# Kernel tuning notes

Measured on AMD Instinct MI355X. Metric: run time of the kernel, lower is better.

## Reference

```python
import jax, jax.numpy as jnp
import numpy as np

N = 50000   # nodes
E = 800000  # edges (avg degree 16)
D = 64      # feature dim (input_dim == hidden_dim == output_dim for num_layer=2)
BN_EPS = 1e-5


def setup_inputs() -> dict:
    key = jax.random.key(0)
    ks = jax.random.split(key, 8)
    def lin_w(k, fan_in, fan_out):
        return jax.random.normal(k, (fan_in, fan_out), jnp.float32) / np.sqrt(fan_in).astype(np.float32)
    inp = {
        "x": jax.random.normal(ks[0], (N, D), jnp.float32),
        "edge_index": jax.random.randint(ks[1], (2, E), 0, N),
    }
    ki = 2
    for l in range(2):
        for s in ("a", "b"):
            inp[f"w{l}{s}"] = lin_w(ks[ki], D, D)
            inp[f"b{l}{s}"] = jnp.zeros((D,), jnp.float32)
            inp[f"g{l}{s}"] = jnp.ones((D,), jnp.float32)   # BN gamma
            inp[f"be{l}{s}"] = jnp.zeros((D,), jnp.float32)  # BN beta
            ki += 1
    inp["lin_w"] = lin_w(ks[6], 2 * D, D)  # JK cat of 2 layers -> 2D, final lin -> D
    inp["lin_b"] = jnp.zeros((D,), jnp.float32)
    return inp


def _bn(h, g, b):
    # BatchNorm1d in training mode: batch statistics over the node axis
    m = h.mean(axis=0)
    v = h.var(axis=0)
    return (h - m) * jax.lax.rsqrt(v + BN_EPS) * g + b


def _gin(h, src, dst, w1, b1, g1, be1, w2, b2, g2, be2):
    # GINConv with eps=0: (1+eps)*x_i + sum_{j->i} x_j, then MLP(Lin-BN-ReLU-Lin-BN-ReLU)
    agg = jax.ops.segment_sum(h[src], dst, num_segments=N) + h
    h = jax.nn.relu(_bn(agg @ w1 + b1, g1, be1))
    return jax.nn.relu(_bn(h @ w2 + b2, g2, be2))


def reference(x, edge_index, w0a, b0a, g0a, be0a, w0b, b0b, g0b, be0b,
              w1a, b1a, g1a, be1a, w1b, b1b, g1b, be1b, lin_w, lin_b):
    src, dst = edge_index[0], edge_index[1]
    h1 = _gin(x, src, dst, w0a, b0a, g0a, be0a, w0b, b0b, g0b, be0b)
    h2 = _gin(h1, src, dst, w1a, b1a, g1a, be1a, w1b, b1b, g1b, be1b)
    # JumpingKnowledge 'cat' over the conv outputs (res[1:]), then final linear
    return jnp.concatenate([h1, h2], axis=1) @ lin_w + lin_b
```

## Files before the change

kernel.cpp:

```cpp
#include <hip/hip_runtime.h>
#include <hip/hip_bf16.h>

#define NN 50000
#define NE 800000
#define BN_EPS 1e-5f
#define CHUNK 8192
#define NCH 98
#define NBK 196

typedef __attribute__((ext_vector_type(4))) float f32x4;
typedef __attribute__((ext_vector_type(4))) short s16x4;

__device__ __forceinline__ float bf2f(__hip_bfloat16 v) { return __bfloat162float(v); }

__global__ void zero_k(int* __restrict__ p, int n) {
    int i = blockIdx.x * 256 + threadIdx.x;
    if (i < n) p[i] = 0;
}

__global__ void cvt_k(const float* __restrict__ X, __hip_bfloat16* __restrict__ Xb) {
    int i = blockIdx.x * 256 + threadIdx.x;
    if (i < NN * 16) {
        f32x4 v = *(const f32x4*)(X + (size_t)i * 4);
        s16x4 ov;
        #pragma unroll
        for (int j = 0; j < 4; j++) {
            __hip_bfloat16 b = __float2bfloat16(v[j]);
            ov[j] = __builtin_bit_cast(short, b);
        }
        *(s16x4*)((short*)Xb + (size_t)i * 4) = ov;
    }
}

__global__ void bhist_k(const int* __restrict__ dst, int* __restrict__ bcnt) {
    __shared__ int c[256];
    int t = threadIdx.x;
    c[t] = 0;
    __syncthreads();
    int base = blockIdx.x * CHUNK;
    int n = NE - base; if (n > CHUNK) n = CHUNK;
    for (int i = t; i < n; i += 256) atomicAdd(&c[dst[base + i] >> 8], 1);
    __syncthreads();
    if (c[t]) atomicAdd(&bcnt[t], c[t]);
}

__global__ void bscan_k(const int* __restrict__ bcnt, int* __restrict__ bbase,
                        int* __restrict__ bres, int* __restrict__ off) {
    __shared__ int s[256];
    int t = threadIdx.x;
    int v = bcnt[t];
    s[t] = v;
    __syncthreads();
    for (int d = 1; d < 256; d <<= 1) {
        int u = (t >= d) ? s[t - d] : 0;
        __syncthreads();
        s[t] += u;
        __syncthreads();
    }
    int ex = s[t] - v;
    bbase[t] = ex;
    bres[t] = ex;
    if (t == 0) { bbase[256] = NE; off[NN] = NE; }
}

__global__ void bscatter_k(const int* __restrict__ src, const int* __restrict__ dst,
                           int* __restrict__ bres, int* __restrict__ ebuf) {
    __shared__ int cnt[256], loff[256], lcur[256], gst[256], sc[256];
    __shared__ int packed[CHUNK];
    int t = threadIdx.x;
    cnt[t] = 0;
    __syncthreads();
    int base = blockIdx.x * CHUNK;
    int n = NE - base; if (n > CHUNK) n = CHUNK;
    for (int i = t; i < n; i += 256) atomicAdd(&cnt[dst[base + i] >> 8], 1);
    __syncthreads();
    sc[t] = cnt[t];
    __syncthreads();
    for (int d = 1; d < 256; d <<= 1) {
        int u = (t >= d) ? sc[t - d] : 0;
        __syncthreads();
        sc[t] += u;
        __syncthreads();
    }
    loff[t] = sc[t] - cnt[t];
    lcur[t] = loff[t];
    __syncthreads();
    for (int i = t; i < n; i += 256) {
        int d = dst[base + i];
        int b = d >> 8;
        int p = atomicAdd(&lcur[b], 1);
        packed[p] = src[base + i] | ((d & 255) << 16) | (b << 24);
    }
    __syncthreads();
    if (cnt[t]) gst[t] = atomicAdd(&bres[t], cnt[t]);
    __syncthreads();
    for (int i = t; i < n; i += 256) {
        int v = packed[i];
        int b = (v >> 24) & 255;
        ebuf[gst[b] + i - loff[b]] = v & 0xFFFFFF;
    }
}

__global__ void csr_k(const int* __restrict__ bbase, const int* __restrict__ ebuf,
                      int* __restrict__ off, int* __restrict__ adj) {
    __shared__ int cnt[256], loff[256], lcur[256], sc[256];
    int b = blockIdx.x, t = threadIdx.x;
    int s0 = bbase[b], s1 = bbase[b + 1];
    int n = s1 - s0;
    cnt[t] = 0;
    __syncthreads();
    for (int i = t; i < n; i += 256) atomicAdd(&cnt[(ebuf[s0 + i] >> 16) & 255], 1);
    __syncthreads();
    sc[t] = cnt[t];
    __syncthreads();
    for (int d = 1; d < 256; d <<= 1) {
        int u = (t >= d) ? sc[t - d] : 0;
        __syncthreads();
        sc[t] += u;
        __syncthreads();
    }
    loff[t] = sc[t] - cnt[t];
    lcur[t] = loff[t];
    int node = b * 256 + t;
    if (node < NN) off[node] = s0 + loff[t];
    __syncthreads();
    for (int i = t; i < n; i += 256) {
        int v = ebuf[s0 + i];
        int p = atomicAdd(&lcur[(v >> 16) & 255], 1);
        adj[s0 + p] = v & 0xFFFF;
    }
}

__global__ void gather_k(const __hip_bfloat16* __restrict__ X,
                         const int* __restrict__ off, const int* __restrict__ adj,
                         float* __restrict__ AGG) {
    int node = blockIdx.x * 4 + (threadIdx.x >> 6);
    int lane = threadIdx.x & 63;
    if (node >= NN) return;
    float acc = bf2f(X[(size_t)node * 64 + lane]);
    int s = off[node], e = off[node + 1];
    int p = s;
    for (; p + 8 <= e; p += 8) {
        int j0 = adj[p + 0], j1 = adj[p + 1], j2 = adj[p + 2], j3 = adj[p + 3];
        int j4 = adj[p + 4], j5 = adj[p + 5], j6 = adj[p + 6], j7 = adj[p + 7];
        float v0 = bf2f(X[(size_t)j0 * 64 + lane]);
        float v1 = bf2f(X[(size_t)j1 * 64 + lane]);
        float v2 = bf2f(X[(size_t)j2 * 64 + lane]);
        float v3 = bf2f(X[(size_t)j3 * 64 + lane]);
        float v4 = bf2f(X[(size_t)j4 * 64 + lane]);
        float v5 = bf2f(X[(size_t)j5 * 64 + lane]);
        float v6 = bf2f(X[(size_t)j6 * 64 + lane]);
        float v7 = bf2f(X[(size_t)j7 * 64 + lane]);
        acc += ((v0 + v1) + (v2 + v3)) + ((v4 + v5) + (v6 + v7));
    }
    if (p + 4 <= e) {
        int j0 = adj[p + 0], j1 = adj[p + 1], j2 = adj[p + 2], j3 = adj[p + 3];
        float v0 = bf2f(X[(size_t)j0 * 64 + lane]);
        float v1 = bf2f(X[(size_t)j1 * 64 + lane]);
        float v2 = bf2f(X[(size_t)j2 * 64 + lane]);
        float v3 = bf2f(X[(size_t)j3 * 64 + lane]);
        acc += (v0 + v1) + (v2 + v3);
        p += 4;
    }
    for (; p < e; p++) acc += bf2f(X[(size_t)adj[p] * 64 + lane]);
    AGG[(size_t)node * 64 + lane] = acc;
}

__global__ void gemm64_k(const float* __restrict__ A,
                         const float* __restrict__ W,
                         const float* __restrict__ bias,
                         float* __restrict__ T,
                         float* __restrict__ sums) {
    __shared__ float As[64 * 72];
    __shared__ float Ws[64 * 64];
    __shared__ float lsum[64], lssq[64];
    int tid = threadIdx.x;
    int rowbase = blockIdx.x * 64;
    for (int i = tid; i < 64 * 16; i += 256) {
        int r = i >> 4, kq = i & 15;
        int row = rowbase + r;
        if (row >= NN) row = NN - 1;
        f32x4 v = *(const f32x4*)(A + (size_t)row * 64 + kq * 4);
        #pragma unroll
        for (int q = 0; q < 4; q++) As[(kq * 4 + q) * 72 + r] = v[q];
    }
    for (int i = tid; i < 1024; i += 256) {
        *(f32x4*)(Ws + i * 4) = *(const f32x4*)(W + i * 4);
    }
    if (tid < 64) { lsum[tid] = 0.f; lssq[tid] = 0.f; }
    __syncthreads();

    int ty = tid >> 4, tx = tid & 15;
    float acc[4][4] = {};
    for (int k = 0; k < 64; k++) {
        float a[4], wv[4];
        #pragma unroll
        for (int i = 0; i < 4; i++) a[i] = As[k * 72 + ty * 4 + i];
        #pragma unroll
        for (int j = 0; j < 4; j++) wv[j] = Ws[k * 64 + tx * 4 + j];
        #pragma unroll
        for (int i = 0; i < 4; i++)
            #pragma unroll
            for (int j = 0; j < 4; j++) acc[i][j] += a[i] * wv[j];
    }

    f32x4 bv = *(const f32x4*)(bias + tx * 4);
    float ps[4] = {0.f, 0.f, 0.f, 0.f}, pq[4] = {0.f, 0.f, 0.f, 0.f};
    #pragma unroll
    for (int i = 0; i < 4; i++) {
        int row = rowbase + ty * 4 + i;
        if (row < NN) {
            f32x4 v;
            #pragma unroll
            for (int j = 0; j < 4; j++) {
                v[j] = acc[i][j] + bv[j];
                ps[j] += v[j];
                pq[j] += v[j] * v[j];
            }
            *(f32x4*)(T + (size_t)row * 64 + tx * 4) = v;
        }
    }
    #pragma unroll
    for (int j = 0; j < 4; j++) {
        atomicAdd(&lsum[tx * 4 + j], ps[j]);
        atomicAdd(&lssq[tx * 4 + j], pq[j]);
    }
    __syncthreads();
    if (tid < 64) {
        atomicAdd(&sums[tid], lsum[tid]);
        atomicAdd(&sums[64 + tid], lssq[tid]);
    }
}

__global__ void gemm64bn_k(const float* __restrict__ Tin,
                           const float* __restrict__ stats,
                           const float* __restrict__ g,
                           const float* __restrict__ be,
                           const float* __restrict__ W,
                           const float* __restrict__ bias,
                           float* __restrict__ T,
                           float* __restrict__ sums) {
    __shared__ float As[64 * 72];
    __shared__ float Ws[64 * 64];
    __shared__ float sc[64], sh[64];
    __shared__ float lsum[64], lssq[64];
    int tid = threadIdx.x;
    int rowbase = blockIdx.x * 64;
    if (tid < 64) {
        float m = stats[tid] * (1.0f / NN);
        float var = stats[64 + tid] * (1.0f / NN) - m * m;
        if (var < 0.f) var = 0.f;
        float s = g[tid] * rsqrtf(var + BN_EPS);
        sc[tid] = s;
        sh[tid] = be[tid] - m * s;
        lsum[tid] = 0.f;
        lssq[tid] = 0.f;
    }
    __syncthreads();
    for (int i = tid; i < 64 * 16; i += 256) {
        int r = i >> 4, kq = i & 15;
        int row = rowbase + r;
        if (row >= NN) row = NN - 1;
        f32x4 v = *(const f32x4*)(Tin + (size_t)row * 64 + kq * 4);
        #pragma unroll
        for (int q = 0; q < 4; q++) {
            int k = kq * 4 + q;
            float u = v[q] * sc[k] + sh[k];
            As[k * 72 + r] = u > 0.f ? u : 0.f;
        }
    }
    for (int i = tid; i < 1024; i += 256) {
        *(f32x4*)(Ws + i * 4) = *(const f32x4*)(W + i * 4);
    }
    __syncthreads();

    int ty = tid >> 4, tx = tid & 15;
    float acc[4][4] = {};
    for (int k = 0; k < 64; k++) {
        float a[4], wv[4];
        #pragma unroll
        for (int i = 0; i < 4; i++) a[i] = As[k * 72 + ty * 4 + i];
        #pragma unroll
        for (int j = 0; j < 4; j++) wv[j] = Ws[k * 64 + tx * 4 + j];
        #pragma unroll
        for (int i = 0; i < 4; i++)
            #pragma unroll
            for (int j = 0; j < 4; j++) acc[i][j] += a[i] * wv[j];
    }

    f32x4 bv = *(const f32x4*)(bias + tx * 4);
    float ps[4] = {0.f, 0.f, 0.f, 0.f}, pq[4] = {0.f, 0.f, 0.f, 0.f};
    #pragma unroll
    for (int i = 0; i < 4; i++) {
        int row = rowbase + ty * 4 + i;
        if (row < NN) {
            f32x4 v;
            #pragma unroll
            for (int j = 0; j < 4; j++) {
                v[j] = acc[i][j] + bv[j];
                ps[j] += v[j];
                pq[j] += v[j] * v[j];
            }
            *(f32x4*)(T + (size_t)row * 64 + tx * 4) = v;
        }
    }
    #pragma unroll
    for (int j = 0; j < 4; j++) {
        atomicAdd(&lsum[tx * 4 + j], ps[j]);
        atomicAdd(&lssq[tx * 4 + j], pq[j]);
    }
    __syncthreads();
    if (tid < 64) {
        atomicAdd(&sums[tid], lsum[tid]);
        atomicAdd(&sums[64 + tid], lssq[tid]);
    }
}

__global__ void bn_k(const float* __restrict__ T, const float* __restrict__ sums,
                     const float* __restrict__ g,
                     const float* __restrict__ be,
                     float* __restrict__ H, __hip_bfloat16* __restrict__ Hb) {
    __shared__ float sc[64], sh[64];
    int tid = threadIdx.x;
    if (tid < 64) {
        float m = sums[tid] * (1.0f / NN);
        float var = sums[64 + tid] * (1.0f / NN) - m * m;
        if (var < 0.f) var = 0.f;
        float s = g[tid] * rsqrtf(var + BN_EPS);
        sc[tid] = s;
        sh[tid] = be[tid] - m * s;
    }
    __syncthreads();
    int i = blockIdx.x * 256 + tid;
    if (i < NN * 16) {
        int row = i >> 4, f = (i & 15) * 4;
        f32x4 v = *(const f32x4*)(T + (size_t)row * 64 + f);
        f32x4 u;
        s16x4 ub;
        #pragma unroll
        for (int j = 0; j < 4; j++) {
            float w = v[j] * sc[f + j] + sh[f + j];
            u[j] = w > 0.f ? w : 0.f;
            __hip_bfloat16 b = __float2bfloat16(u[j]);
            ub[j] = __builtin_bit_cast(short, b);
        }
        *(f32x4*)(H + (size_t)row * 64 + f) = u;
        *(s16x4*)((short*)Hb + (size_t)row * 64 + f) = ub;
    }
}

__global__ void gemmfin2_k(const float* __restrict__ H1,
                           const float* __restrict__ T2,
                           const float* __restrict__ stats,
                           const float* __restrict__ g,
                           const float* __restrict__ be,
                           const float* __restrict__ W,
                           const float* __restrict__ bias,
                           float* __restrict__ O) {
    __shared__ float As[128 * 72];
    __shared__ float Ws[128 * 64];
    __shared__ float sc[64], sh[64];
    int tid = threadIdx.x;
    int rowbase = blockIdx.x * 64;
    if (tid < 64) {
        float m = stats[tid] * (1.0f / NN);
        float var = stats[64 + tid] * (1.0f / NN) - m * m;
        if (var < 0.f) var = 0.f;
        float s = g[tid] * rsqrtf(var + BN_EPS);
        sc[tid] = s;
        sh[tid] = be[tid] - m * s;
    }
    __syncthreads();
    for (int i = tid; i < 64 * 16; i += 256) {
        int r = i >> 4, kq = i & 15;
        int row = rowbase + r;
        if (row >= NN) row = NN - 1;
        f32x4 v1 = *(const f32x4*)(H1 + (size_t)row * 64 + kq * 4);
        f32x4 v2 = *(const f32x4*)(T2 + (size_t)row * 64 + kq * 4);
        #pragma unroll
        for (int q = 0; q < 4; q++) {
            int k = kq * 4 + q;
            As[k * 72 + r] = v1[q];
            float u = v2[q] * sc[k] + sh[k];
            As[(64 + k) * 72 + r] = u > 0.f ? u : 0.f;
        }
    }
    for (int i = tid; i < 2048; i += 256) {
        *(f32x4*)(Ws + i * 4) = *(const f32x4*)(W + i * 4);
    }
    __syncthreads();

    int ty = tid >> 4, tx = tid & 15;
    float acc[4][4] = {};
    for (int k = 0; k < 128; k++) {
        float a[4], wv[4];
        #pragma unroll
        for (int i = 0; i < 4; i++) a[i] = As[k * 72 + ty * 4 + i];
        #pragma unroll
        for (int j = 0; j < 4; j++) wv[j] = Ws[k * 64 + tx * 4 + j];
        #pragma unroll
        for (int i = 0; i < 4; i++)
            #pragma unroll
            for (int j = 0; j < 4; j++) acc[i][j] += a[i] * wv[j];
    }

    f32x4 bv = *(const f32x4*)(bias + tx * 4);
    #pragma unroll
    for (int i = 0; i < 4; i++) {
        int row = rowbase + ty * 4 + i;
        if (row < NN) {
            f32x4 v;
            #pragma unroll
            for (int j = 0; j < 4; j++) v[j] = acc[i][j] + bv[j];
            *(f32x4*)(O + (size_t)row * 64 + tx * 4) = v;
        }
    }
}

extern "C" void kernel_launch(void* const* d_in, const int* in_sizes, int n_in,
                              void* d_out, int out_size, void* d_ws, size_t ws_size,
                              hipStream_t stream) {
    const float* x   = (const float*)d_in[0];
    const int*   ei  = (const int*)d_in[1];
    const float* w0a = (const float*)d_in[2];
    const float* b0a = (const float*)d_in[3];
    const float* g0a = (const float*)d_in[4];
    const float* be0a= (const float*)d_in[5];
    const float* w0b = (const float*)d_in[6];
    const float* b0b = (const float*)d_in[7];
    const float* g0b = (const float*)d_in[8];
    const float* be0b= (const float*)d_in[9];
    const float* w1a = (const float*)d_in[10];
    const float* b1a = (const float*)d_in[11];
    const float* g1a = (const float*)d_in[12];
    const float* be1a= (const float*)d_in[13];
    const float* w1b = (const float*)d_in[14];
    const float* b1b = (const float*)d_in[15];
    const float* g1b = (const float*)d_in[16];
    const float* be1b= (const float*)d_in[17];
    const float* lw  = (const float*)d_in[18];
    const float* lb  = (const float*)d_in[19];
    float* out = (float*)d_out;
    (void)in_sizes; (void)n_in; (void)out_size; (void)ws_size;

    char* wsb = (char*)d_ws;
    size_t o = 0;
    auto alloc = [&](size_t bytes) -> char* {
        char* p = wsb + o;
        o += (bytes + 255) & ~(size_t)255;
        return p;
    };
    int* bcnt = (int*)alloc(256 * 4);
    float* sums = (float*)alloc(512 * 4);
    int* bbase = (int*)alloc(257 * 4);
    int* bres = (int*)alloc(256 * 4);
    int* off = (int*)alloc((NN + 1) * 4);
    int* adj = (int*)alloc(NE * 4);
    int* ebuf = (int*)alloc(NE * 4);
    float* AGG = (float*)alloc((size_t)NN * 64 * 4);
    float* T   = (float*)alloc((size_t)NN * 64 * 4);
    float* T2  = (float*)alloc((size_t)NN * 64 * 4);
    float* HC  = (float*)alloc((size_t)NN * 64 * 4);
    __hip_bfloat16* Xb  = (__hip_bfloat16*)alloc((size_t)NN * 64 * 2);
    __hip_bfloat16* HCb = (__hip_bfloat16*)alloc((size_t)NN * 64 * 2);

    const int* src = ei;
    const int* dst = ei + NE;

    zero_k<<<3, 256, 0, stream>>>((int*)d_ws, 768);
    bhist_k<<<NCH, 256, 0, stream>>>(dst, bcnt);
    bscan_k<<<1, 256, 0, stream>>>(bcnt, bbase, bres, off);
    bscatter_k<<<NCH, 256, 0, stream>>>(src, dst, bres, ebuf);
    csr_k<<<NBK, 256, 0, stream>>>(bbase, ebuf, off, adj);

    const int ggrid = NN / 4;
    const int mgrid = (NN + 63) / 64;
    const int agrid = (NN * 16 + 255) / 256;

    cvt_k<<<agrid, 256, 0, stream>>>(x, Xb);

    gather_k<<<ggrid, 256, 0, stream>>>(Xb, off, adj, AGG);
    gemm64_k<<<mgrid, 256, 0, stream>>>(AGG, w0a, b0a, T, sums + 0);
    gemm64bn_k<<<mgrid, 256, 0, stream>>>(T, sums + 0, g0a, be0a, w0b, b0b, T2, sums + 128);
    bn_k<<<agrid, 256, 0, stream>>>(T2, sums + 128, g0b, be0b, HC, HCb);

    gather_k<<<ggrid, 256, 0, stream>>>(HCb, off, adj, AGG);
    gemm64_k<<<mgrid, 256, 0, stream>>>(AGG, w1a, b1a, T, sums + 256);
    gemm64bn_k<<<mgrid, 256, 0, stream>>>(T, sums + 256, g1a, be1a, w1b, b1b, T2, sums + 384);

    gemmfin2_k<<<mgrid, 256, 0, stream>>>(HC, T2, sums + 384, g1b, be1b, lw, lb, out);
}
```

Baseline: 355.2 us.

## Use bf16 MFMA for dense GEMMs and merge preprocessing kernels

Replaces the fp32 LDS-tiled GEMMs with bf16 MFMA 16x16x32 instructions that read operands directly from global memory, using weights pre-transposed to bf16. The aggregation output and the layer-1 hidden state are stored in bf16 instead of fp32, which cuts memory traffic. Histogram, feature conversion and weight conversion are merged into one prep kernel with per-chunk partial counts, which removes the zeroing kernel and the global atomics. The cost is lower precision in the GEMM inputs, and the output stores are now scalar and strided rather than vectorized.

```diff
diff --git a/kernel.cpp b/kernel.cpp
--- a/kernel.cpp
+++ b/kernel.cpp
@@ -4,51 +4,72 @@
 #define NN 50000
 #define NE 800000
 #define BN_EPS 1e-5f
-#define CHUNK 8192
-#define NCH 98
+#define CHUNK 4096
+#define NCH 196
 #define NBK 196
 
 typedef __attribute__((ext_vector_type(4))) float f32x4;
+typedef __attribute__((ext_vector_type(8))) short s16x8;
 typedef __attribute__((ext_vector_type(4))) short s16x4;
 
 __device__ __forceinline__ float bf2f(__hip_bfloat16 v) { return __bfloat162float(v); }
-
-__global__ void zero_k(int* __restrict__ p, int n) {
-    int i = blockIdx.x * 256 + threadIdx.x;
-    if (i < n) p[i] = 0;
-}
-
-__global__ void cvt_k(const float* __restrict__ X, __hip_bfloat16* __restrict__ Xb) {
-    int i = blockIdx.x * 256 + threadIdx.x;
-    if (i < NN * 16) {
-        f32x4 v = *(const f32x4*)(X + (size_t)i * 4);
-        s16x4 ov;
-        #pragma unroll
-        for (int j = 0; j < 4; j++) {
-            __hip_bfloat16 b = __float2bfloat16(v[j]);
-            ov[j] = __builtin_bit_cast(short, b);
-        }
-        *(s16x4*)((short*)Xb + (size_t)i * 4) = ov;
-    }
-}
-
-__global__ void bhist_k(const int* __restrict__ dst, int* __restrict__ bcnt) {
-    __shared__ int c[256];
-    int t = threadIdx.x;
-    c[t] = 0;
-    __syncthreads();
-    int base = blockIdx.x * CHUNK;
-    int n = NE - base; if (n > CHUNK) n = CHUNK;
-    for (int i = t; i < n; i += 256) atomicAdd(&c[dst[base + i] >> 8], 1);
-    __syncthreads();
-    if (c[t]) atomicAdd(&bcnt[t], c[t]);
-}
-
-__global__ void bscan_k(const int* __restrict__ bcnt, int* __restrict__ bbase,
-                        int* __restrict__ bres, int* __restrict__ off) {
+__device__ __forceinline__ short f2bs(float v) {
+    __hip_bfloat16 b = __float2bfloat16(v);
+    return __builtin_bit_cast(short, b);
+}
+
+__global__ void prep_k(const int* __restrict__ dst, int* __restrict__ part,
+                       const float* __restrict__ x, __hip_bfloat16* __restrict__ Xb,
+                       const float* __restrict__ w0a, const float* __restrict__ w0b,
+                       const float* __restrict__ w1a, const float* __restrict__ w1b,
+                       const float* __restrict__ lw,
+                       short* __restrict__ Wt0a, short* __restrict__ Wt0b,
+                       short* __restrict__ Wt1a, short* __restrict__ Wt1b,
+                       short* __restrict__ Wtf) {
+    int b = blockIdx.x, t = threadIdx.x;
+    if (b < NCH) {
+        __shared__ int c[256];
+        c[t] = 0;
+        __syncthreads();
+        int base = b * CHUNK;
+        int n = NE - base; if (n > CHUNK) n = CHUNK;
+        for (int i = t; i < n; i += 256) atomicAdd(&c[dst[base + i] >> 8], 1);
+        __syncthreads();
+        part[b * 256 + t] = c[t];
+    } else if (b < 196 + 3125) {
+        int i = (b - 196) * 256 + t;
+        if (i < NN * 16) {
+            f32x4 v = *(const f32x4*)(x + (size_t)i * 4);
+            s16x4 ov;
+            #pragma unroll
+            for (int j = 0; j < 4; j++) ov[j] = f2bs(v[j]);
+            *(s16x4*)((short*)Xb + (size_t)i * 4) = ov;
+        }
+    } else {
+        int wb = b - 3321;
+        if (wb < 4) {
+            const float* W = wb == 0 ? w0a : wb == 1 ? w0b : wb == 2 ? w1a : w1b;
+            short* Wt = wb == 0 ? Wt0a : wb == 1 ? Wt0b : wb == 2 ? Wt1a : Wt1b;
+            for (int e = t; e < 4096; e += 256) {
+                int k = e >> 6, n = e & 63;
+                Wt[n * 64 + k] = f2bs(W[e]);
+            }
+        } else {
+            for (int e = t; e < 8192; e += 256) {
+                int k = e >> 6, n = e & 63;
+                Wtf[n * 128 + k] = f2bs(lw[e]);
+            }
+        }
+    }
+}
+
+__global__ void bscan_k(const int* __restrict__ part, int* __restrict__ bbase,
+                        int* __restrict__ bres, int* __restrict__ off,
+                        float* __restrict__ sums) {
     __shared__ int s[256];
     int t = threadIdx.x;
-    int v = bcnt[t];
+    int v = 0;
+    for (int c = 0; c < NCH; c++) v += part[c * 256 + t];
     s[t] = v;
     __syncthreads();
     for (int d = 1; d < 256; d <<= 1) {
@@ -61,6 +82,7 @@
     bbase[t] = ex;
     bres[t] = ex;
     if (t == 0) { bbase[256] = NE; off[NN] = NE; }
+    sums[t] = 0.f; sums[256 + t] = 0.f;
 }
 
 __global__ void bscatter_k(const int* __restrict__ src, const int* __restrict__ dst,
@@ -133,7 +155,7 @@
 
 __global__ void gather_k(const __hip_bfloat16* __restrict__ X,
                          const int* __restrict__ off, const int* __restrict__ adj,
-                         float* __restrict__ AGG) {
+                         __hip_bfloat16* __restrict__ AGG) {
     int node = blockIdx.x * 4 + (threadIdx.x >> 6);
     int lane = threadIdx.x & 63;
     if (node >= NN) return;
@@ -163,67 +185,54 @@
         p += 4;
     }
     for (; p < e; p++) acc += bf2f(X[(size_t)adj[p] * 64 + lane]);
-    AGG[(size_t)node * 64 + lane] = acc;
-}
-
-__global__ void gemm64_k(const float* __restrict__ A,
-                         const float* __restrict__ W,
+    AGG[(size_t)node * 64 + lane] = __float2bfloat16(acc);
+}
+
+
+__global__ void gemm_a_k(const __hip_bfloat16* __restrict__ Ab,
+                         const short* __restrict__ Wt,
                          const float* __restrict__ bias,
                          float* __restrict__ T,
                          float* __restrict__ sums) {
-    __shared__ float As[64 * 72];
-    __shared__ float Ws[64 * 64];
     __shared__ float lsum[64], lssq[64];
     int tid = threadIdx.x;
-    int rowbase = blockIdx.x * 64;
-    for (int i = tid; i < 64 * 16; i += 256) {
-        int r = i >> 4, kq = i & 15;
-        int row = rowbase + r;
-        if (row >= NN) row = NN - 1;
-        f32x4 v = *(const f32x4*)(A + (size_t)row * 64 + kq * 4);
+    if (tid < 64) { lsum[tid] = 0.f; lssq[tid] = 0.f; }
+    __syncthreads();
+    int wv = tid >> 6, L = tid & 63;
+    int m = L & 15, quad = L >> 4;
+    int wrow = blockIdx.x * 64 + wv * 16;
+    int arow = wrow + m;
+    if (arow >= NN) arow = NN - 1;
+    const short* Ap = (const short*)Ab;
+    s16x8 a0 = *(const s16x8*)(Ap + (size_t)arow * 64 + quad * 8);
+    s16x8 a1 = *(const s16x8*)(Ap + (size_t)arow * 64 + 32 + quad * 8);
+    f32x4 acc[4];
+    #pragma unroll
+    for (int nt = 0; nt < 4; nt++) {
+        int n = nt * 16 + m;
+        s16x8 b0 = *(const s16x8*)(Wt + n * 64 + quad * 8);
+        s16x8 b1 = *(const s16x8*)(Wt + n * 64 + 32 + quad * 8);
+        acc[nt] = (f32x4){0.f, 0.f, 0.f, 0.f};
+        acc[nt] = __builtin_amdgcn_mfma_f32_16x16x32_bf16(a0, b0, acc[nt], 0, 0, 0);
+        acc[nt] = __builtin_amdgcn_mfma_f32_16x16x32_bf16(a1, b1, acc[nt], 0, 0, 0);
+    }
+    #pragma unroll
+    for (int nt = 0; nt < 4; nt++) {
+        int col = nt * 16 + m;
+        float bv = bias[col];
+        float ps = 0.f, pq = 0.f;
         #pragma unroll
-        for (int q = 0; q < 4; q++) As[(kq * 4 + q) * 72 + r] = v[q];
-    }
-    for (int i = tid; i < 1024; i += 256) {
-        *(f32x4*)(Ws + i * 4) = *(const f32x4*)(W + i * 4);
-    }
-    if (tid < 64) { lsum[tid] = 0.f; lssq[tid] = 0.f; }
-    __syncthreads();
-
-    int ty = tid >> 4, tx = tid & 15;
-    float acc[4][4] = {};
-    for (int k = 0; k < 64; k++) {
-        float a[4], wv[4];
-        #pragma unroll
-        for (int i = 0; i < 4; i++) a[i] = As[k * 72 + ty * 4 + i];
-        #pragma unroll
-        for (int j = 0; j < 4; j++) wv[j] = Ws[k * 64 + tx * 4 + j];
-        #pragma unroll
-        for (int i = 0; i < 4; i++)
-            #pragma unroll
-            for (int j = 0; j < 4; j++) acc[i][j] += a[i] * wv[j];
-    }
-
-    f32x4 bv = *(const f32x4*)(bias + tx * 4);
-    float ps[4] = {0.f, 0.f, 0.f, 0.f}, pq[4] = {0.f, 0.f, 0.f, 0.f};
-    #pragma unroll
-    for (int i = 0; i < 4; i++) {
-        int row = rowbase + ty * 4 + i;
-        if (row < NN) {
-            f32x4 v;
-            #pragma unroll
-            for (int j = 0; j < 4; j++) {
-                v[j] = acc[i][j] + bv[j];
-                ps[j] += v[j];
-                pq[j] += v[j] * v[j];
+        for (int r = 0; r < 4; r++) {
+            int orow = wrow + quad * 4 + r;
+            if (orow < NN) {
+                float v = acc[nt][r] + bv;
+                T[(size_t)orow * 64 + col] = v;
+                ps += v;
+                pq += v * v;
             }
-            *(f32x4*)(T + (size_t)row * 64 + tx * 4) = v;
-        }
-    }
-    #pragma unroll
-    for (int j = 0; j < 4; j++) {
-        atomicAdd(&lsum[tx * 4 + j], ps[j]);
-        atomicAdd(&lssq[tx * 4 + j], pq[j]);
+        }
+        atomicAdd(&lsum[col], ps);
+        atomicAdd(&lssq[col], pq);
     }
     __syncthreads();
     if (tid < 64) {
@@ -232,82 +241,70 @@
     }
 }
 
-__global__ void gemm64bn_k(const float* __restrict__ Tin,
-                           const float* __restrict__ stats,
-                           const float* __restrict__ g,
-                           const float* __restrict__ be,
-                           const float* __restrict__ W,
-                           const float* __restrict__ bias,
-                           float* __restrict__ T,
-                           float* __restrict__ sums) {
-    __shared__ float As[64 * 72];
-    __shared__ float Ws[64 * 64];
-    __shared__ float sc[64], sh[64];
-    __shared__ float lsum[64], lssq[64];
+__global__ void gemm_bn_k(const float* __restrict__ Tin,
+                          const float* __restrict__ stats,
+                          const float* __restrict__ g, const float* __restrict__ be,
+                          const short* __restrict__ Wt,
+                          const float* __restrict__ bias,
+                          float* __restrict__ T,
+                          float* __restrict__ sums) {
+    __shared__ float sc[64], sh[64], lsum[64], lssq[64];
     int tid = threadIdx.x;
-    int rowbase = blockIdx.x * 64;
     if (tid < 64) {
-        float m = stats[tid] * (1.0f / NN);
-        float var = stats[64 + tid] * (1.0f / NN) - m * m;
+        float mm = stats[tid] * (1.0f / NN);
+        float var = stats[64 + tid] * (1.0f / NN) - mm * mm;
         if (var < 0.f) var = 0.f;
         float s = g[tid] * rsqrtf(var + BN_EPS);
         sc[tid] = s;
-        sh[tid] = be[tid] - m * s;
-        lsum[tid] = 0.f;
-        lssq[tid] = 0.f;
-    }
-    __syncthreads();
-    for (int i = tid; i < 64 * 16; i += 256) {
-        int r = i >> 4, kq = i & 15;
-        int row = rowbase + r;
-        if (row >= NN) row = NN - 1;
-        f32x4 v = *(const f32x4*)(Tin + (size_t)row * 64 + kq * 4);
+        sh[tid] = be[tid] - mm * s;
+        lsum[tid] = 0.f; lssq[tid] = 0.f;
+    }
+    __syncthreads();
+    int wv = tid >> 6, L = tid & 63;
+    int m = L & 15, quad = L >> 4;
+    int wrow = blockIdx.x * 64 + wv * 16;
+    int arow = wrow + m;
+    if (arow >= NN) arow = NN - 1;
+    f32x4 t0 = *(const f32x4*)(Tin + (size_t)arow * 64 + quad * 8);
+    f32x4 t1 = *(const f32x4*)(Tin + (size_t)arow * 64 + quad * 8 + 4);
+    f32x4 t2 = *(const f32x4*)(Tin + (size_t)arow * 64 + 32 + quad * 8);
+    f32x4 t3 = *(const f32x4*)(Tin + (size_t)arow * 64 + 32 + quad * 8 + 4);
+    s16x8 a0, a1;
+    #pragma unroll
+    for (int j = 0; j < 4; j++) {
+        int k0 = quad * 8 + j, k1 = quad * 8 + 4 + j;
+        float u0 = t0[j] * sc[k0] + sh[k0]; a0[j]     = f2bs(u0 > 0.f ? u0 : 0.f);
+        float u1 = t1[j] * sc[k1] + sh[k1]; a0[4 + j] = f2bs(u1 > 0.f ? u1 : 0.f);
+        float u2 = t2[j] * sc[32 + k0] + sh[32 + k0]; a1[j]     = f2bs(u2 > 0.f ? u2 : 0.f);
+        float u3 = t3[j] * sc[32 + k1] + sh[32 + k1]; a1[4 + j] = f2bs(u3 > 0.f ? u3 : 0.f);
+    }
+    f32x4 acc[4];
+    #pragma unroll
+    for (int nt = 0; nt < 4; nt++) {
+        int n = nt * 16 + m;
+        s16x8 b0 = *(const s16x8*)(Wt + n * 64 + quad * 8);
+        s16x8 b1 = *(const s16x8*)(Wt + n * 64 + 32 + quad * 8);
+        acc[nt] = (f32x4){0.f, 0.f, 0.f, 0.f};
+        acc[nt] = __builtin_amdgcn_mfma_f32_16x16x32_bf16(a0, b0, acc[nt], 0, 0, 0);
+        acc[nt] = __builtin_amdgcn_mfma_f32_16x16x32_bf16(a1, b1, acc[nt], 0, 0, 0);
+    }
+    #pragma unroll
+    for (int nt = 0; nt < 4; nt++) {
+        int col = nt * 16 + m;
+        float bv = bias[col];
+        float ps = 0.f, pq = 0.f;
         #pragma unroll
-        for (int q = 0; q < 4; q++) {
-            int k = kq * 4 + q;
-            float u = v[q] * sc[k] + sh[k];
-            As[k * 72 + r] = u > 0.f ? u : 0.f;
-        }
-    }
-    for (int i = tid; i < 1024; i += 256) {
-        *(f32x4*)(Ws + i * 4) = *(const f32x4*)(W + i * 4);
-    }
-    __syncthreads();
-
-    int ty = tid >> 4, tx = tid & 15;
-    float acc[4][4] = {};
-    for (int k = 0; k < 64; k++) {
-        float a[4], wv[4];
-        #pragma unroll
-        for (int i = 0; i < 4; i++) a[i] = As[k * 72 + ty * 4 + i];
-        #pragma unroll
-        for (int j = 0; j < 4; j++) wv[j] = Ws[k * 64 + tx * 4 + j];
-        #pragma unroll
-        for (int i = 0; i < 4; i++)
-            #pragma unroll
-            for (int j = 0; j < 4; j++) acc[i][j] += a[i] * wv[j];
-    }
-
-    f32x4 bv = *(const f32x4*)(bias + tx * 4);
-    float ps[4] = {0.f, 0.f, 0.f, 0.f}, pq[4] = {0.f, 0.f, 0.f, 0.f};
-    #pragma unroll
-    for (int i = 0; i < 4; i++) {
-        int row = rowbase + ty * 4 + i;
-        if (row < NN) {
-            f32x4 v;
-            #pragma unroll
-            for (int j = 0; j < 4; j++) {
-                v[j] = acc[i][j] + bv[j];
-                ps[j] += v[j];
-                pq[j] += v[j] * v[j];
+        for (int r = 0; r < 4; r++) {
+            int orow = wrow + quad * 4 + r;
+            if (orow < NN) {
+                float v = acc[nt][r] + bv;
+                T[(size_t)orow * 64 + col] = v;
+                ps += v;
+                pq += v * v;
             }
-            *(f32x4*)(T + (size_t)row * 64 + tx * 4) = v;
-        }
-    }
-    #pragma unroll
-    for (int j = 0; j < 4; j++) {
-        atomicAdd(&lsum[tx * 4 + j], ps[j]);
-        atomicAdd(&lssq[tx * 4 + j], pq[j]);
+        }
+        atomicAdd(&lsum[col], ps);
+        atomicAdd(&lssq[col], pq);
     }
     __syncthreads();
     if (tid < 64) {
@@ -317,9 +314,8 @@
 }
 
 __global__ void bn_k(const float* __restrict__ T, const float* __restrict__ sums,
-                     const float* __restrict__ g,
-                     const float* __restrict__ be,
-                     float* __restrict__ H, __hip_bfloat16* __restrict__ Hb) {
+                     const float* __restrict__ g, const float* __restrict__ be,
+                     __hip_bfloat16* __restrict__ Hb) {
     __shared__ float sc[64], sh[64];
     int tid = threadIdx.x;
     if (tid < 64) {
@@ -335,84 +331,77 @@
     if (i < NN * 16) {
         int row = i >> 4, f = (i & 15) * 4;
         f32x4 v = *(const f32x4*)(T + (size_t)row * 64 + f);
-        f32x4 u;
         s16x4 ub;
         #pragma unroll
         for (int j = 0; j < 4; j++) {
             float w = v[j] * sc[f + j] + sh[f + j];
-            u[j] = w > 0.f ? w : 0.f;
-            __hip_bfloat16 b = __float2bfloat16(u[j]);
-            ub[j] = __builtin_bit_cast(short, b);
-        }
-        *(f32x4*)(H + (size_t)row * 64 + f) = u;
+            ub[j] = f2bs(w > 0.f ? w : 0.f);
+        }
         *(s16x4*)((short*)Hb + (size_t)row * 64 + f) = ub;
     }
 }
 
-__global__ void gemmfin2_k(const float* __restrict__ H1,
+__global__ void gemm_fin_k(const __hip_bfloat16* __restrict__ H1b,
                            const float* __restrict__ T2,
                            const float* __restrict__ stats,
-                           const float* __restrict__ g,
-                           const float* __restrict__ be,
-                           const float* __restrict__ W,
+                           const float* __restrict__ g, const float* __restrict__ be,
+                           const short* __restrict__ Wtf,
                            const float* __restrict__ bias,
                            float* __restrict__ O) {
-    __shared__ float As[128 * 72];
-    __shared__ float Ws[128 * 64];
     __shared__ float sc[64], sh[64];
     int tid = threadIdx.x;
-    int rowbase = blockIdx.x * 64;
     if (tid < 64) {
-        float m = stats[tid] * (1.0f / NN);
-        float var = stats[64 + tid] * (1.0f / NN) - m * m;
+        float mm = stats[tid] * (1.0f / NN);
+        float var = stats[64 + tid] * (1.0f / NN) - mm * mm;
         if (var < 0.f) var = 0.f;
         float s = g[tid] * rsqrtf(var + BN_EPS);
         sc[tid] = s;
-        sh[tid] = be[tid] - m * s;
-    }
-    __syncthreads();
-    for (int i = tid; i < 64 * 16; i += 256) {
-        int r = i >> 4, kq = i & 15;
-        int row = rowbase + r;
-        if (row >= NN) row = NN - 1;
-        f32x4 v1 = *(const f32x4*)(H1 + (size_t)row * 64 + kq * 4);
-        f32x4 v2 = *(const f32x4*)(T2 + (size_t)row * 64 + kq * 4);
+        sh[tid] = be[tid] - mm * s;
+    }
+    __syncthreads();
+    int wv = tid >> 6, L = tid & 63;
+    int m = L & 15, quad = L >> 4;
+    int wrow = blockIdx.x * 64 + wv * 16;
+    int arow = wrow + m;
+    if (arow >= NN) arow = NN - 1;
+    const short* Hp = (const short*)H1b;
+    s16x8 a0 = *(const s16x8*)(Hp + (size_t)arow * 64 + quad * 8);
+    s16x8 a1 = *(const s16x8*)(Hp + (size_t)arow * 64 + 32 + quad * 8);
+    f32x4 t0 = *(const f32x4*)(T2 + (size_t)arow * 64 + quad * 8);
+    f32x4 t1 = *(const f32x4*)(T2 + (size_t)arow * 64 + quad * 8 + 4);
+    f32x4 t2 = *(const f32x4*)(T2 + (size_t)arow * 64 + 32 + quad * 8);
+    f32x4 t3 = *(const f32x4*)(T2 + (size_t)arow * 64 + 32 + quad * 8 + 4);
+    s16x8 a2, a3;
+    #pragma unroll
+    for (int j = 0; j < 4; j++) {
+        int k0 = quad * 8 + j, k1 = quad * 8 + 4 + j;
+        float u0 = t0[j] * sc[k0] + sh[k0]; a2[j]     = f2bs(u0 > 0.f ? u0 : 0.f);
+        float u1 = t1[j] * sc[k1] + sh[k1]; a2[4 + j] = f2bs(u1 > 0.f ? u1 : 0.f);
+        float u2 = t2[j] * sc[32 + k0] + sh[32 + k0]; a3[j]     = f2bs(u2 > 0.f ? u2 : 0.f);
+        float u3 = t3[j] * sc[32 + k1] + sh[32 + k1]; a3[4 + j] = f2bs(u3 > 0.f ? u3 : 0.f);
+    }
+    f32x4 acc[4];
+    #pragma unroll
+    for (int nt = 0; nt < 4; nt++) {
+        int n = nt * 16 + m;
+        s16x8 b0 = *(const s16x8*)(Wtf + n * 128 + quad * 8);
+        s16x8 b1 = *(const s16x8*)(Wtf + n * 128 + 32 + quad * 8);
+        s16x8 b2 = *(const s16x8*)(Wtf + n * 128 + 64 + quad * 8);
+        s16x8 b3 = *(const s16x8*)(Wtf + n * 128 + 96 + quad * 8);
+        acc[nt] = (f32x4){0.f, 0.f, 0.f, 0.f};
+        acc[nt] = __builtin_amdgcn_mfma_f32_16x16x32_bf16(a0, b0, acc[nt], 0, 0, 0);
+        acc[nt] = __builtin_amdgcn_mfma_f32_16x16x32_bf16(a1, b1, acc[nt], 0, 0, 0);
+        acc[nt] = __builtin_amdgcn_mfma_f32_16x16x32_bf16(a2, b2, acc[nt], 0, 0, 0);
+        acc[nt] = __builtin_amdgcn_mfma_f32_16x16x32_bf16(a3, b3, acc[nt], 0, 0, 0);
+    }
+    #pragma unroll
+    for (int nt = 0; nt < 4; nt++) {
+        int col = nt * 16 + m;
+        float bv = bias[col];
         #pragma unroll
-        for (int q = 0; q < 4; q++) {
-            int k = kq * 4 + q;
-            As[k * 72 + r] = v1[q];
-            float u = v2[q] * sc[k] + sh[k];
-            As[(64 + k) * 72 + r] = u > 0.f ? u : 0.f;
-        }
-    }
-    for (int i = tid; i < 2048; i += 256) {
-        *(f32x4*)(Ws + i * 4) = *(const f32x4*)(W + i * 4);
-    }
-    __syncthreads();
-
-    int ty = tid >> 4, tx = tid & 15;
-    float acc[4][4] = {};
-    for (int k = 0; k < 128; k++) {
-        float a[4], wv[4];
-        #pragma unroll
-        for (int i = 0; i < 4; i++) a[i] = As[k * 72 + ty * 4 + i];
-        #pragma unroll
-        for (int j = 0; j < 4; j++) wv[j] = Ws[k * 64 + tx * 4 + j];
-        #pragma unroll
-        for (int i = 0; i < 4; i++)
-            #pragma unroll
-            for (int j = 0; j < 4; j++) acc[i][j] += a[i] * wv[j];
-    }
-
-    f32x4 bv = *(const f32x4*)(bias + tx * 4);
-    #pragma unroll
-    for (int i = 0; i < 4; i++) {
-        int row = rowbase + ty * 4 + i;
-        if (row < NN) {
-            f32x4 v;
-            #pragma unroll
-            for (int j = 0; j < 4; j++) v[j] = acc[i][j] + bv[j];
-            *(f32x4*)(O + (size_t)row * 64 + tx * 4) = v;
+        for (int r = 0; r < 4; r++) {
+            int orow = wrow + quad * 4 + r;
+            if (orow < NN) O[(size_t)orow * 64 + col] = acc[nt][r] + bv;
         }
     }
 }
@@ -450,26 +439,30 @@
         o += (bytes + 255) & ~(size_t)255;
         return p;
     };
-    int* bcnt = (int*)alloc(256 * 4);
+    int* part = (int*)alloc(NCH * 256 * 4);
     float* sums = (float*)alloc(512 * 4);
     int* bbase = (int*)alloc(257 * 4);
     int* bres = (int*)alloc(256 * 4);
     int* off = (int*)alloc((NN + 1) * 4);
     int* adj = (int*)alloc(NE * 4);
     int* ebuf = (int*)alloc(NE * 4);
-    float* AGG = (float*)alloc((size_t)NN * 64 * 4);
-    float* T   = (float*)alloc((size_t)NN * 64 * 4);
-    float* T2  = (float*)alloc((size_t)NN * 64 * 4);
-    float* HC  = (float*)alloc((size_t)NN * 64 * 4);
-    __hip_bfloat16* Xb  = (__hip_bfloat16*)alloc((size_t)NN * 64 * 2);
-    __hip_bfloat16* HCb = (__hip_bfloat16*)alloc((size_t)NN * 64 * 2);
+    __hip_bfloat16* Xb   = (__hip_bfloat16*)alloc((size_t)NN * 64 * 2);
+    __hip_bfloat16* AGGb = (__hip_bfloat16*)alloc((size_t)NN * 64 * 2);
+    __hip_bfloat16* HCb  = (__hip_bfloat16*)alloc((size_t)NN * 64 * 2);
+    float* T  = (float*)alloc((size_t)NN * 64 * 4);
+    float* T2 = (float*)alloc((size_t)NN * 64 * 4);
+    short* Wt0a = (short*)alloc(4096 * 2);
+    short* Wt0b = (short*)alloc(4096 * 2);
+    short* Wt1a = (short*)alloc(4096 * 2);
+    short* Wt1b = (short*)alloc(4096 * 2);
+    short* Wtf  = (short*)alloc(8192 * 2);
 
     const int* src = ei;
     const int* dst = ei + NE;
 
-    zero_k<<<3, 256, 0, stream>>>((int*)d_ws, 768);
-    bhist_k<<<NCH, 256, 0, stream>>>(dst, bcnt);
-    bscan_k<<<1, 256, 0, stream>>>(bcnt, bbase, bres, off);
+    prep_k<<<3326, 256, 0, stream>>>(dst, part, x, Xb, w0a, w0b, w1a, w1b, lw,
+                                     Wt0a, Wt0b, Wt1a, Wt1b, Wtf);
+    bscan_k<<<1, 256, 0, stream>>>(part, bbase, bres, off, sums);
     bscatter_k<<<NCH, 256, 0, stream>>>(src, dst, bres, ebuf);
     csr_k<<<NBK, 256, 0, stream>>>(bbase, ebuf, off, adj);
 
@@ -477,16 +470,14 @@
     const int mgrid = (NN + 63) / 64;
     const int agrid = (NN * 16 + 255) / 256;
 
-    cvt_k<<<agrid, 256, 0, stream>>>(x, Xb);
-
-    gather_k<<<ggrid, 256, 0, stream>>>(Xb, off, adj, AGG);
-    gemm64_k<<<mgrid, 256, 0, stream>>>(AGG, w0a, b0a, T, sums + 0);
-    gemm64bn_k<<<mgrid, 256, 0, stream>>>(T, sums + 0, g0a, be0a, w0b, b0b, T2, sums + 128);
-    bn_k<<<agrid, 256, 0, stream>>>(T2, sums + 128, g0b, be0b, HC, HCb);
-
-    gather_k<<<ggrid, 256, 0, stream>>>(HCb, off, adj, AGG);
-    gemm64_k<<<mgrid, 256, 0, stream>>>(AGG, w1a, b1a, T, sums + 256);
-    gemm64bn_k<<<mgrid, 256, 0, stream>>>(T, sums + 256, g1a, be1a, w1b, b1b, T2, sums + 384);
-
-    gemmfin2_k<<<mgrid, 256, 0, stream>>>(HC, T2, sums + 384, g1b, be1b, lw, lb, out);
-}
+    gather_k<<<ggrid, 256, 0, stream>>>(Xb, off, adj, AGGb);
+    gemm_a_k<<<mgrid, 256, 0, stream>>>(AGGb, Wt0a, b0a, T, sums + 0);
+    gemm_bn_k<<<mgrid, 256, 0, stream>>>(T, sums + 0, g0a, be0a, Wt0b, b0b, T2, sums + 128);
+    bn_k<<<agrid, 256, 0, stream>>>(T2, sums + 128, g0b, be0b, HCb);
+
+    gather_k<<<ggrid, 256, 0, stream>>>(HCb, off, adj, AGGb);
+    gemm_a_k<<<mgrid, 256, 0, stream>>>(AGGb, Wt1a, b1a, T, sums + 256);
+    gemm_bn_k<<<mgrid, 256, 0, stream>>>(T, sums + 256, g1a, be1a, Wt1b, b1b, T2, sums + 384);
+
+    gemm_fin_k<<<mgrid, 256, 0, stream>>>(HCb, T2, sums + 384, g1b, be1b, Wtf, lb, out);
+}
```

Measured after the change: 348.3 us. No clear change (-1.9%).
